# Optimization experiments

Measured on AMD Instinct MI355X. Metric: run time of the kernel, lower is better.

The kernel has to match this reference:

```python
import jax, jax.numpy as jnp
import numpy as np

GAMMA = 2.0  # init arg gamma
EPS = 1e-8   # torch F.cosine_similarity eps


def setup_inputs() -> dict:
    key = jax.random.key(0)
    k1, k2, k3 = jax.random.split(key, 3)
    B, C, H, W_ = 4, 256, 64, 64
    x = jax.random.normal(k1, (B, C, H, W_), dtype=jnp.float32)
    # 1x1 conv weight [out_c, in_c] and bias
    W = jax.random.normal(k2, (C, C), dtype=jnp.float32) * (1.0 / np.sqrt(C))
    b = jax.random.normal(k3, (C,), dtype=jnp.float32) * 0.01
    return {"x": x, "W": W, "b": b}


def reference(x, W, b):
    B, C, H, W_ = x.shape
    N = H * W_
    xf = x.reshape(B, C, N)                                    # [B,C,N]
    # cosine similarity across channel dim, with torch-style eps clamp
    norm = jnp.maximum(jnp.sqrt(jnp.sum(xf * xf, axis=1)), EPS)  # [B,N]
    xn = xf / norm[:, None, :]                                  # [B,C,N]
    sim = jnp.einsum('bcn,bcm->bnm', xn, xn)                    # [B,N,N]
    sim = jax.nn.relu(sim) ** GAMMA
    # 1x1 conv = per-pixel channel mixing
    t = jnp.einsum('oc,bchw->bohw', W, x) + b[None, :, None, None]
    tf = t.reshape(B, C, N)                                     # [B,C,N]
    # einsum 'b x y h w, b c h w -> b c x y'
    out = jnp.einsum('bnm,bcm->bcn', sim, tf)
    return out.reshape(B, C, H, W_)
```

## Files before the change

### kernel.cpp

```cpp
#include <hip/hip_runtime.h>
#include <stdint.h>

#define CC 256
#define NN 4096

typedef __attribute__((ext_vector_type(8))) short short8;
typedef __attribute__((ext_vector_type(4))) float floatx4;
typedef __attribute__((ext_vector_type(4))) unsigned int uint4v;
typedef __attribute__((ext_vector_type(2))) unsigned int uint2v;

__device__ __forceinline__ unsigned short f2bf(float f) {
    unsigned int u = __builtin_bit_cast(unsigned int, f);
    u = (u + 0x7FFFu + ((u >> 16) & 1u)) >> 16;
    return (unsigned short)u;
}

__device__ __forceinline__ floatx4 mfma16(short8 a, short8 b, floatx4 c) {
    return __builtin_amdgcn_mfma_f32_16x16x32_bf16(a, b, c, 0, 0, 0);
}

__device__ __forceinline__ int swz8(int row, int g) {
    return row * 256 + (((g ^ (row & 7)) & 31) << 3);
}

__global__ __launch_bounds__(256) void k_wcast(const float* __restrict__ Wm,
                                               unsigned short* __restrict__ wbf) {
    int i = blockIdx.x * 256 + threadIdx.x;
    floatx4 v = *(const floatx4*)(Wm + (size_t)i * 4);
    unsigned int a = f2bf(v[0]) | ((unsigned int)f2bf(v[1]) << 16);
    unsigned int b = f2bf(v[2]) | ((unsigned int)f2bf(v[3]) << 16);
    uint2v p = {a, b};
    *(uint2v*)(wbf + (size_t)i * 4) = p;
}

__global__ __launch_bounds__(256) void k_trans(const float* __restrict__ x,
                                               unsigned short* __restrict__ xT,
                                               float* __restrict__ psum) {
    int blk = blockIdx.x;
    int b  = blk >> 8;
    int cc = (blk >> 6) & 3;
    int nc = blk & 63;
    int c0 = cc << 6, n0 = nc << 6;
    __shared__ float tile[64][65];
    __shared__ float red[4][64];
    int t = threadIdx.x;
    {
        int c   = t >> 2;
        int nn4 = (t & 3) << 4;
        const float* src = x + (size_t)(b * CC + c0 + c) * NN + n0 + nn4;
        #pragma unroll
        for (int j = 0; j < 16; j += 4) {
            floatx4 v = *(const floatx4*)(src + j);
            tile[c][nn4 + j + 0] = v[0];
            tile[c][nn4 + j + 1] = v[1];
            tile[c][nn4 + j + 2] = v[2];
            tile[c][nn4 + j + 3] = v[3];
        }
    }
    __syncthreads();
    {
        int n  = t >> 2;
        int ci = (t & 3) << 4;
        unsigned short* dst = xT + (size_t)(b * NN + n0 + n) * CC + c0 + ci;
        unsigned int w[8];
        #pragma unroll
        for (int j = 0; j < 8; ++j) {
            unsigned int lo = f2bf(tile[ci + 2 * j][n]);
            unsigned int hi = f2bf(tile[ci + 2 * j + 1][n]);
            w[j] = lo | (hi << 16);
        }
        uint4v w0 = {w[0], w[1], w[2], w[3]};
        uint4v w1 = {w[4], w[5], w[6], w[7]};
        *(uint4v*)(dst)     = w0;
        *(uint4v*)(dst + 8) = w1;
    }
    {
        int n  = t & 63;
        int cq = t >> 6;
        float ss = 0.f;
        #pragma unroll
        for (int i = 0; i < 16; ++i) {
            float v = tile[cq * 16 + i][n];
            ss = fmaf(v, v, ss);
        }
        red[cq][n] = ss;
    }
    __syncthreads();
    if (t < 64) {
        float s = red[0][t] + red[1][t] + red[2][t] + red[3][t];
        psum[((size_t)(b * 64 + nc) * 64 + t) * 4 + cc] = s;
    }
}

__global__ __launch_bounds__(256) void k_inv(const float* __restrict__ psum,
                                             float* __restrict__ invn) {
    int i = blockIdx.x * 256 + threadIdx.x;
    floatx4 p = *(const floatx4*)(psum + (size_t)i * 4);
    float ss = (p[0] + p[1]) + (p[2] + p[3]);
    invn[i] = 1.f / fmaxf(sqrtf(ss), 1e-8f);
}

__global__ __launch_bounds__(256) void k_conv(const unsigned short* __restrict__ wbf,
                                              const float* __restrict__ bias,
                                              const unsigned short* __restrict__ xT,
                                              unsigned short* __restrict__ tfF) {
    int blk = blockIdx.x;
    int b = blk >> 6, nt = blk & 63;
    int n0 = nt << 6;
    int t = threadIdx.x;
    int w = t >> 6, l15 = t & 15, q = (t & 63) >> 4;

    __shared__ unsigned short xm[64 * 256];
    const unsigned short* xTb = xT + (size_t)b * NN * CC;

    #pragma unroll
    for (int j = 0; j < 8; ++j) {
        int grow = j * 8 + (t >> 5);
        int g = t & 31;
        uint4v v = *(const uint4v*)(xTb + (size_t)(n0 + grow) * CC + g * 8);
        *(uint4v*)(xm + swz8(grow, g)) = v;
    }
    __syncthreads();

    floatx4 zero4 = {0.f, 0.f, 0.f, 0.f};
    floatx4 acc[4][4];
    #pragma unroll
    for (int ot = 0; ot < 4; ++ot)
        #pragma unroll
        for (int ns = 0; ns < 4; ++ns) acc[ot][ns] = zero4;

    #pragma unroll
    for (int kk = 0; kk < 8; ++kk) {
        short8 aw[4], bx[4];
        #pragma unroll
        for (int ot = 0; ot < 4; ++ot)
            aw[ot] = *(const short8*)(wbf + (size_t)(64 * w + 16 * ot + l15) * CC + kk * 32 + q * 8);
        #pragma unroll
        for (int ns = 0; ns < 4; ++ns)
            bx[ns] = *(const short8*)(xm + swz8(16 * ns + l15, kk * 4 + q));
        #pragma unroll
        for (int ot = 0; ot < 4; ++ot)
            #pragma unroll
            for (int ns = 0; ns < 4; ++ns)
                acc[ot][ns] = mfma16(aw[ot], bx[ns], acc[ot][ns]);
    }

    unsigned short* dst = tfF + (size_t)(b * 64 + nt) * 16 * 1024;
    #pragma unroll
    for (int ot = 0; ot < 4; ++ot) {
        int ct = 4 * w + ot;
        float bv[4];
        #pragma unroll
        for (int i = 0; i < 4; ++i) bv[i] = bias[16 * ct + q * 4 + i];
        #pragma unroll
        for (int ns = 0; ns < 4; ++ns)
            #pragma unroll
            for (int i = 0; i < 4; ++i) {
                int mloc = 16 * ns + l15;
                int kk2 = mloc >> 5, qp = (mloc >> 3) & 3, j = mloc & 7;
                int lanep = qp * 16 + (q * 4 + i);
                dst[ct * 1024 + kk2 * 512 + lanep * 8 + j] = f2bf(acc[ot][ns][i] + bv[i]);
            }
    }
}

__global__ __launch_bounds__(512, 2) void k_fused(
        const unsigned short* __restrict__ xT,
        const unsigned short* __restrict__ tfF,
        const float* __restrict__ invn,
        float* __restrict__ out) {
    int blk = blockIdx.x;
    int b  = blk >> 6;
    int n0 = (blk & 63) << 6;
    int t  = threadIdx.x;
    int wv = t >> 6;
    int l15 = t & 15, q = (t & 63) >> 4;
    int ms = wv & 3;
    int np = wv >> 2;

    __shared__ unsigned short xm[64 * 256];
    __shared__ unsigned short pbuf[4][16 * 72];

    const unsigned short* xTb = xT + (size_t)b * NN * CC;
    const unsigned short* tFb = tfF + (size_t)b * 64 * 16 * 1024;
    const float* invb = invn + b * NN;

    short8 aq[2][8];
    #pragma unroll
    for (int s = 0; s < 2; ++s) {
        const unsigned short* p = xTb + (size_t)(n0 + 16 * (2 * np + s) + l15) * CC + q * 8;
        #pragma unroll
        for (int kk = 0; kk < 8; ++kk) aq[s][kk] = *(const short8*)(p + kk * 32);
    }
    float invq[2][4];
    #pragma unroll
    for (int s = 0; s < 2; ++s)
        #pragma unroll
        for (int i = 0; i < 4; ++i)
            invq[s][i] = invb[n0 + 16 * (2 * np + s) + q * 4 + i];

    floatx4 zero4 = {0.f, 0.f, 0.f, 0.f};
    floatx4 oacc[2][4];
    #pragma unroll
    for (int ci = 0; ci < 2; ++ci)
        #pragma unroll
        for (int nqs = 0; nqs < 4; ++nqs) oacc[ci][nqs] = zero4;

    int srow = t >> 5;
    int sg   = t & 31;

    uint4v gx[4];
    #pragma unroll
    for (int j = 0; j < 4; ++j)
        gx[j] = *(const uint4v*)(xTb + (size_t)(j * 16 + srow) * CC + sg * 8);
    #pragma unroll
    for (int j = 0; j < 4; ++j)
        *(uint4v*)(xm + swz8(j * 16 + srow, sg)) = gx[j];
    __syncthreads();

    for (int it = 0; it < 64; ++it) {
        int m0 = it << 6;
        int m1 = (it < 63 ? (it + 1) : 63) << 6;
        #pragma unroll
        for (int j = 0; j < 4; ++j)
            gx[j] = *(const uint4v*)(xTb + (size_t)(m1 + j * 16 + srow) * CC + sg * 8);
        short8 tfr[2][2];
        #pragma unroll
        for (int kk2 = 0; kk2 < 2; ++kk2)
            #pragma unroll
            for (int ci = 0; ci < 2; ++ci) {
                int ct = wv + 8 * ci;
                tfr[kk2][ci] = *(const short8*)(tFb + (size_t)(it * 16 + ct) * 1024
                                                + kk2 * 512 + (t & 63) * 8);
            }
        float invm = invb[m0 + 16 * ms + l15];

        short8 bq[8];
        #pragma unroll
        for (int kk = 0; kk < 8; ++kk)
            bq[kk] = *(const short8*)(xm + swz8(16 * ms + l15, kk * 4 + q));
        floatx4 s0a = zero4, s0b = zero4, s1a = zero4, s1b = zero4;
        #pragma unroll
        for (int kk = 0; kk < 8; kk += 2) {
            s0a = mfma16(aq[0][kk],     bq[kk],     s0a);
            s1a = mfma16(aq[1][kk],     bq[kk],     s1a);
            s0b = mfma16(aq[0][kk + 1], bq[kk + 1], s0b);
            s1b = mfma16(aq[1][kk + 1], bq[kk + 1], s1b);
        }
        #pragma unroll
        for (int s = 0; s < 2; ++s) {
            floatx4 sv = (s == 0) ? (s0a + s0b) : (s1a + s1b);
            unsigned short* pw = &pbuf[2 * np + s][16 * ms + l15];
            #pragma unroll
            for (int i = 0; i < 4; ++i) {
                float v = sv[i] * (invq[s][i] * invm);
                v = fmaxf(v, 0.f);
                v = v * v;
                pw[(q * 4 + i) * 72] = f2bf(v);
            }
        }
        asm volatile("s_waitcnt lgkmcnt(0)\n\ts_barrier" ::: "memory");

        #pragma unroll
        for (int kk2 = 0; kk2 < 2; ++kk2) {
            #pragma unroll
            for (int nqs = 0; nqs < 4; ++nqs) {
                short8 pb = *(const short8*)(&pbuf[nqs][l15 * 72 + kk2 * 32 + q * 8]);
                oacc[0][nqs] = mfma16(tfr[kk2][0], pb, oacc[0][nqs]);
                oacc[1][nqs] = mfma16(tfr[kk2][1], pb, oacc[1][nqs]);
            }
        }
        #pragma unroll
        for (int j = 0; j < 4; ++j)
            *(uint4v*)(xm + swz8(j * 16 + srow, sg)) = gx[j];
        asm volatile("s_waitcnt lgkmcnt(0)\n\ts_barrier" ::: "memory");
    }

    float* ob = out + (size_t)b * CC * NN;
    #pragma unroll
    for (int ci = 0; ci < 2; ++ci) {
        int ct = wv + 8 * ci;
        #pragma unroll
        for (int nqs = 0; nqs < 4; ++nqs)
            #pragma unroll
            for (int i = 0; i < 4; ++i) {
                int c = 16 * ct + q * 4 + i;
                ob[(size_t)c * NN + n0 + 16 * nqs + l15] = oacc[ci][nqs][i];
            }
    }
}

extern "C" void kernel_launch(void* const* d_in, const int* in_sizes, int n_in,
                              void* d_out, int out_size, void* d_ws, size_t ws_size,
                              hipStream_t stream) {
    const float* x    = (const float*)d_in[0];
    const float* Wm   = (const float*)d_in[1];
    const float* bias = (const float*)d_in[2];
    float* out = (float*)d_out;

    char* ws = (char*)d_ws;
    float* psum         = (float*)ws;
    float* invn         = (float*)(ws + 262144);
    unsigned short* xT  = (unsigned short*)(ws + 262144 + 65536);
    unsigned short* wbf = (unsigned short*)(ws + 262144 + 65536 + 8388608);
    unsigned short* tfF = (unsigned short*)(ws + 262144 + 65536 + 8388608 + 131072);

    k_wcast<<<64,   256, 0, stream>>>(Wm, wbf);
    k_trans<<<1024, 256, 0, stream>>>(x, xT, psum);
    k_inv  <<<64,   256, 0, stream>>>(psum, invn);
    k_conv <<<256,  256, 0, stream>>>(wbf, bias, xT, tfF);
    k_fused<<<256,  512, 0, stream>>>(xT, tfF, invn, out);
}
```

Before: 174.0 us.

## Reassociate conv after similarity matmul, applying W and bias in epilogue

Instead of computing the 1x1 conv t=Wx+b before the similarity-weighted sum, the fused kernel accumulates Z = x·simᵀ using pre-fragmented bf16 x tiles, tracks the row sums of sim, and then applies W·Z plus bias times row sum in an epilogue GEMM. This removes the separate conv kernel and its output round-trip, replacing it with a cheap fragment-layout shuffle kernel. It adds extra LDS for staging Z, which may reduce occupancy, and introduces an extra bf16 rounding of Z.

```diff
diff --git a/kernel.cpp b/kernel.cpp
--- a/kernel.cpp
+++ b/kernel.cpp
@@ -24,13 +24,20 @@
 }
 
 __global__ __launch_bounds__(256) void k_wcast(const float* __restrict__ Wm,
-                                               unsigned short* __restrict__ wbf) {
-    int i = blockIdx.x * 256 + threadIdx.x;
-    floatx4 v = *(const floatx4*)(Wm + (size_t)i * 4);
-    unsigned int a = f2bf(v[0]) | ((unsigned int)f2bf(v[1]) << 16);
-    unsigned int b = f2bf(v[2]) | ((unsigned int)f2bf(v[3]) << 16);
-    uint2v p = {a, b};
-    *(uint2v*)(wbf + (size_t)i * 4) = p;
+                                               unsigned short* __restrict__ wF) {
+    int idx = blockIdx.x * 256 + threadIdx.x;
+    int f = idx >> 6, lane = idx & 63;
+    int ct = f >> 3, kk = f & 7;
+    int l15 = lane & 15, q = lane >> 4;
+    const float* src = Wm + (size_t)(16 * ct + l15) * CC + 32 * kk + 8 * q;
+    floatx4 a = *(const floatx4*)src;
+    floatx4 c = *(const floatx4*)(src + 4);
+    unsigned int w0 = f2bf(a[0]) | ((unsigned int)f2bf(a[1]) << 16);
+    unsigned int w1 = f2bf(a[2]) | ((unsigned int)f2bf(a[3]) << 16);
+    unsigned int w2 = f2bf(c[0]) | ((unsigned int)f2bf(c[1]) << 16);
+    unsigned int w3 = f2bf(c[2]) | ((unsigned int)f2bf(c[3]) << 16);
+    uint4v p = {w0, w1, w2, w3};
+    *(uint4v*)(wF + (size_t)f * 512 + lane * 8) = p;
 }
 
 __global__ __launch_bounds__(256) void k_trans(const float* __restrict__ x,
@@ -100,73 +107,46 @@
     invn[i] = 1.f / fmaxf(sqrtf(ss), 1e-8f);
 }
 
-__global__ __launch_bounds__(256) void k_conv(const unsigned short* __restrict__ wbf,
-                                              const float* __restrict__ bias,
-                                              const unsigned short* __restrict__ xT,
-                                              unsigned short* __restrict__ tfF) {
+__global__ __launch_bounds__(256) void k_gfrag(const unsigned short* __restrict__ xT,
+                                               unsigned short* __restrict__ xG) {
     int blk = blockIdx.x;
-    int b = blk >> 6, nt = blk & 63;
-    int n0 = nt << 6;
+    int b = blk >> 6, mt = blk & 63;
+    __shared__ unsigned short tile[64 * 264];
     int t = threadIdx.x;
-    int w = t >> 6, l15 = t & 15, q = (t & 63) >> 4;
-
-    __shared__ unsigned short xm[64 * 256];
-    const unsigned short* xTb = xT + (size_t)b * NN * CC;
-
+    const unsigned short* src = xT + (size_t)(b * NN + mt * 64) * CC;
     #pragma unroll
     for (int j = 0; j < 8; ++j) {
-        int grow = j * 8 + (t >> 5);
-        int g = t & 31;
-        uint4v v = *(const uint4v*)(xTb + (size_t)(n0 + grow) * CC + g * 8);
-        *(uint4v*)(xm + swz8(grow, g)) = v;
-    }
-    __syncthreads();
-
-    floatx4 zero4 = {0.f, 0.f, 0.f, 0.f};
-    floatx4 acc[4][4];
-    #pragma unroll
-    for (int ot = 0; ot < 4; ++ot)
-        #pragma unroll
-        for (int ns = 0; ns < 4; ++ns) acc[ot][ns] = zero4;
-
-    #pragma unroll
-    for (int kk = 0; kk < 8; ++kk) {
-        short8 aw[4], bx[4];
-        #pragma unroll
-        for (int ot = 0; ot < 4; ++ot)
-            aw[ot] = *(const short8*)(wbf + (size_t)(64 * w + 16 * ot + l15) * CC + kk * 32 + q * 8);
-        #pragma unroll
-        for (int ns = 0; ns < 4; ++ns)
-            bx[ns] = *(const short8*)(xm + swz8(16 * ns + l15, kk * 4 + q));
-        #pragma unroll
-        for (int ot = 0; ot < 4; ++ot)
-            #pragma unroll
-            for (int ns = 0; ns < 4; ++ns)
-                acc[ot][ns] = mfma16(aw[ot], bx[ns], acc[ot][ns]);
-    }
-
-    unsigned short* dst = tfF + (size_t)(b * 64 + nt) * 16 * 1024;
-    #pragma unroll
-    for (int ot = 0; ot < 4; ++ot) {
-        int ct = 4 * w + ot;
-        float bv[4];
-        #pragma unroll
-        for (int i = 0; i < 4; ++i) bv[i] = bias[16 * ct + q * 4 + i];
-        #pragma unroll
-        for (int ns = 0; ns < 4; ++ns)
-            #pragma unroll
-            for (int i = 0; i < 4; ++i) {
-                int mloc = 16 * ns + l15;
-                int kk2 = mloc >> 5, qp = (mloc >> 3) & 3, j = mloc & 7;
-                int lanep = qp * 16 + (q * 4 + i);
-                dst[ct * 1024 + kk2 * 512 + lanep * 8 + j] = f2bf(acc[ot][ns][i] + bv[i]);
+        int idx = j * 256 + t;
+        int row = idx >> 5, g = idx & 31;
+        uint4v v = *(const uint4v*)(src + (size_t)row * CC + g * 8);
+        *(uint4v*)(tile + row * 264 + g * 8) = v;
+    }
+    __syncthreads();
+    unsigned short* dst = xG + (size_t)(b * 64 + mt) * 16 * 1024;
+    int lane = t & 63, l15 = lane & 15, q = lane >> 4;
+    #pragma unroll
+    for (int cc2 = 0; cc2 < 4; ++cc2) {
+        int cct = (t >> 6) * 4 + cc2;
+        #pragma unroll
+        for (int kk2 = 0; kk2 < 2; ++kk2) {
+            unsigned int w[4];
+            #pragma unroll
+            for (int j2 = 0; j2 < 4; ++j2) {
+                unsigned int lo = tile[(32 * kk2 + 8 * q + 2 * j2) * 264 + 16 * cct + l15];
+                unsigned int hi = tile[(32 * kk2 + 8 * q + 2 * j2 + 1) * 264 + 16 * cct + l15];
+                w[j2] = lo | (hi << 16);
             }
+            uint4v p = {w[0], w[1], w[2], w[3]};
+            *(uint4v*)(dst + cct * 1024 + kk2 * 512 + lane * 8) = p;
+        }
     }
 }
 
 __global__ __launch_bounds__(512, 2) void k_fused(
         const unsigned short* __restrict__ xT,
-        const unsigned short* __restrict__ tfF,
+        const unsigned short* __restrict__ xG,
+        const unsigned short* __restrict__ wF,
+        const float* __restrict__ bias,
         const float* __restrict__ invn,
         float* __restrict__ out) {
     int blk = blockIdx.x;
@@ -180,9 +160,11 @@
 
     __shared__ unsigned short xm[64 * 256];
     __shared__ unsigned short pbuf[4][16 * 72];
+    __shared__ unsigned short zbuf[64 * 264];
+    __shared__ float spbuf2[4][64];
 
     const unsigned short* xTb = xT + (size_t)b * NN * CC;
-    const unsigned short* tFb = tfF + (size_t)b * 64 * 16 * 1024;
+    const unsigned short* xGb = xG + (size_t)b * 64 * 16 * 1024;
     const float* invb = invn + b * NN;
 
     short8 aq[2][8];
@@ -200,15 +182,19 @@
             invq[s][i] = invb[n0 + 16 * (2 * np + s) + q * 4 + i];
 
     floatx4 zero4 = {0.f, 0.f, 0.f, 0.f};
-    floatx4 oacc[2][4];
+    floatx4 Zacc[2][4];
     #pragma unroll
     for (int ci = 0; ci < 2; ++ci)
         #pragma unroll
-        for (int nqs = 0; nqs < 4; ++nqs) oacc[ci][nqs] = zero4;
+        for (int nqs = 0; nqs < 4; ++nqs) Zacc[ci][nqs] = zero4;
+    float csum[2][4];
+    #pragma unroll
+    for (int s = 0; s < 2; ++s)
+        #pragma unroll
+        for (int i = 0; i < 4; ++i) csum[s][i] = 0.f;
 
     int srow = t >> 5;
     int sg   = t & 31;
-
     uint4v gx[4];
     #pragma unroll
     for (int j = 0; j < 4; ++j)
@@ -224,14 +210,14 @@
         #pragma unroll
         for (int j = 0; j < 4; ++j)
             gx[j] = *(const uint4v*)(xTb + (size_t)(m1 + j * 16 + srow) * CC + sg * 8);
-        short8 tfr[2][2];
-        #pragma unroll
-        for (int kk2 = 0; kk2 < 2; ++kk2)
-            #pragma unroll
-            for (int ci = 0; ci < 2; ++ci) {
-                int ct = wv + 8 * ci;
-                tfr[kk2][ci] = *(const short8*)(tFb + (size_t)(it * 16 + ct) * 1024
-                                                + kk2 * 512 + (t & 63) * 8);
+        short8 xg[2][2];
+        #pragma unroll
+        for (int ci = 0; ci < 2; ++ci)
+            #pragma unroll
+            for (int kk2 = 0; kk2 < 2; ++kk2) {
+                int cct = wv + 8 * ci;
+                xg[ci][kk2] = *(const short8*)(xGb + (size_t)(it * 16 + cct) * 1024
+                                               + kk2 * 512 + (t & 63) * 8);
             }
         float invm = invb[m0 + 16 * ms + l15];
 
@@ -256,37 +242,89 @@
                 float v = sv[i] * (invq[s][i] * invm);
                 v = fmaxf(v, 0.f);
                 v = v * v;
+                csum[s][i] += v;
                 pw[(q * 4 + i) * 72] = f2bf(v);
             }
         }
         asm volatile("s_waitcnt lgkmcnt(0)\n\ts_barrier" ::: "memory");
 
         #pragma unroll
-        for (int kk2 = 0; kk2 < 2; ++kk2) {
+        for (int kk2 = 0; kk2 < 2; ++kk2)
             #pragma unroll
             for (int nqs = 0; nqs < 4; ++nqs) {
-                short8 pb = *(const short8*)(&pbuf[nqs][l15 * 72 + kk2 * 32 + q * 8]);
-                oacc[0][nqs] = mfma16(tfr[kk2][0], pb, oacc[0][nqs]);
-                oacc[1][nqs] = mfma16(tfr[kk2][1], pb, oacc[1][nqs]);
+                short8 pbf = *(const short8*)(&pbuf[nqs][l15 * 72 + kk2 * 32 + q * 8]);
+                Zacc[0][nqs] = mfma16(xg[0][kk2], pbf, Zacc[0][nqs]);
+                Zacc[1][nqs] = mfma16(xg[1][kk2], pbf, Zacc[1][nqs]);
             }
-        }
         #pragma unroll
         for (int j = 0; j < 4; ++j)
             *(uint4v*)(xm + swz8(j * 16 + srow, sg)) = gx[j];
         asm volatile("s_waitcnt lgkmcnt(0)\n\ts_barrier" ::: "memory");
     }
 
+    #pragma unroll
+    for (int mask = 1; mask < 16; mask <<= 1)
+        #pragma unroll
+        for (int s = 0; s < 2; ++s)
+            #pragma unroll
+            for (int i = 0; i < 4; ++i)
+                csum[s][i] += __shfl_xor(csum[s][i], mask, 64);
+
+    __syncthreads();
+    #pragma unroll
+    for (int ci = 0; ci < 2; ++ci) {
+        int cct = wv + 8 * ci;
+        #pragma unroll
+        for (int nqs = 0; nqs < 4; ++nqs)
+            #pragma unroll
+            for (int i = 0; i < 4; ++i)
+                zbuf[(16 * nqs + l15) * 264 + 16 * cct + 4 * q + i] = f2bf(Zacc[ci][nqs][i]);
+    }
+    if (l15 == 0) {
+        #pragma unroll
+        for (int s = 0; s < 2; ++s)
+            #pragma unroll
+            for (int i = 0; i < 4; ++i)
+                spbuf2[ms][16 * (2 * np + s) + 4 * q + i] = csum[s][i];
+    }
+    __syncthreads();
+
+    float svals[4];
+    #pragma unroll
+    for (int nqs = 0; nqs < 4; ++nqs)
+        svals[nqs] = spbuf2[0][16 * nqs + l15] + spbuf2[1][16 * nqs + l15]
+                   + spbuf2[2][16 * nqs + l15] + spbuf2[3][16 * nqs + l15];
+
     float* ob = out + (size_t)b * CC * NN;
+    floatx4 oa[2][4];
     #pragma unroll
     for (int ci = 0; ci < 2; ++ci) {
         int ct = wv + 8 * ci;
+        floatx4 bv = *(const floatx4*)(bias + 16 * ct + 4 * q);
         #pragma unroll
         for (int nqs = 0; nqs < 4; ++nqs)
             #pragma unroll
-            for (int i = 0; i < 4; ++i) {
-                int c = 16 * ct + q * 4 + i;
-                ob[(size_t)c * NN + n0 + 16 * nqs + l15] = oacc[ci][nqs][i];
-            }
+            for (int i = 0; i < 4; ++i) oa[ci][nqs][i] = bv[i] * svals[nqs];
+    }
+    #pragma unroll
+    for (int kk = 0; kk < 8; ++kk) {
+        short8 wf0 = *(const short8*)(wF + (size_t)(wv * 8 + kk) * 512 + (t & 63) * 8);
+        short8 wf1 = *(const short8*)(wF + (size_t)((wv + 8) * 8 + kk) * 512 + (t & 63) * 8);
+        #pragma unroll
+        for (int nqs = 0; nqs < 4; ++nqs) {
+            short8 zf = *(const short8*)(&zbuf[(16 * nqs + l15) * 264 + 32 * kk + 8 * q]);
+            oa[0][nqs] = mfma16(wf0, zf, oa[0][nqs]);
+            oa[1][nqs] = mfma16(wf1, zf, oa[1][nqs]);
+        }
+    }
+    #pragma unroll
+    for (int ci = 0; ci < 2; ++ci) {
+        int ct = wv + 8 * ci;
+        #pragma unroll
+        for (int nqs = 0; nqs < 4; ++nqs)
+            #pragma unroll
+            for (int i = 0; i < 4; ++i)
+                ob[(size_t)(16 * ct + 4 * q + i) * NN + n0 + 16 * nqs + l15] = oa[ci][nqs][i];
     }
 }
 
@@ -302,12 +340,12 @@
     float* psum         = (float*)ws;
     float* invn         = (float*)(ws + 262144);
     unsigned short* xT  = (unsigned short*)(ws + 262144 + 65536);
-    unsigned short* wbf = (unsigned short*)(ws + 262144 + 65536 + 8388608);
-    unsigned short* tfF = (unsigned short*)(ws + 262144 + 65536 + 8388608 + 131072);
-
-    k_wcast<<<64,   256, 0, stream>>>(Wm, wbf);
+    unsigned short* wF  = (unsigned short*)(ws + 262144 + 65536 + 8388608);
+    unsigned short* xG  = (unsigned short*)(ws + 262144 + 65536 + 8388608 + 131072);
+
+    k_wcast<<<32,   256, 0, stream>>>(Wm, wF);
     k_trans<<<1024, 256, 0, stream>>>(x, xT, psum);
     k_inv  <<<64,   256, 0, stream>>>(psum, invn);
-    k_conv <<<256,  256, 0, stream>>>(wbf, bias, xT, tfF);
-    k_fused<<<256,  512, 0, stream>>>(xT, tfF, invn, out);
-}
+    k_gfrag<<<256,  256, 0, stream>>>(xT, xG);
+    k_fused<<<256,  512, 0, stream>>>(xT, xG, wF, bias, invn, out);
+}
```

Measured after the change: 169.9 us. -2.4%, faster.
